# Optimization experiments

Measured on AMD Instinct MI355X. Metric: run time of the kernel, lower is better.

Reference implementation:

```python
import jax, jax.numpy as jnp
import numpy as np


def setup_inputs() -> dict:
    key = jax.random.key(0)
    k1, k2 = jax.random.split(key)
    N, D, C = 65536, 512, 64
    embeddings = jax.random.normal(k1, (N, D), dtype=jnp.float32)
    labels = jax.random.randint(k2, (N,), 0, C, dtype=jnp.int64)
    return {"embeddings": embeddings, "labels": labels, "num_classes": C}


def reference(embeddings, labels, num_classes):
    # Per-class mean (prototypes) via segment reductions. Labels are assumed
    # to be 0..C-1 with all classes present, so unique(labels) == arange(C)
    # and local_labels == labels (faithful to the torch loop in that regime).
    ones = jnp.ones(labels.shape, dtype=embeddings.dtype)
    counts = jax.ops.segment_sum(ones, labels, num_segments=num_classes)  # [C]
    sums = jax.ops.segment_sum(embeddings, labels, num_segments=num_classes)  # [C, D]
    prototypes = sums / counts[:, None]

    # Euclidean cdist: ||e||^2 + ||p||^2 - 2 e.p^T, clamped for numerical safety
    e2 = jnp.sum(embeddings * embeddings, axis=1, keepdims=True)  # [N, 1]
    p2 = jnp.sum(prototypes * prototypes, axis=1)  # [C]
    cross = embeddings @ prototypes.T  # [N, C]
    d2 = jnp.maximum(e2 + p2[None, :] - 2.0 * cross, 1e-12)
    logits = -jnp.sqrt(d2)  # [N, C], negative distances

    log_probs = jax.nn.log_softmax(logits, axis=1)
    n = labels.shape[0]
    nll = -log_probs[jnp.arange(n), labels]
    loss = jnp.mean(nll)
    accuracy = jnp.mean((jnp.argmax(logits, axis=1) == labels).astype(jnp.float32))
    return (loss, accuracy)
```

## Files before the change

kernel.cpp:

```cpp
#include <hip/hip_runtime.h>
#include <math.h>

#define NROWS 65536
#define DIM   512
#define NCLS  64
#define CCAP  1280

typedef __attribute__((ext_vector_type(4))) float f32x4;
typedef __attribute__((ext_vector_type(8))) short s16x8;

#define WS_PROTOSUM 0
#define WS_CURSORS  32768
#define WS_LOSS     32832
#define WS_ACC      32833
#define WS_DONE     32834
#define WS_P2       32836
#define WS_PERM     32912
#define WS_PBF      114944
#define MEMSET_WORDS 32835

static __device__ __forceinline__ unsigned short f2bf(float f) {
    unsigned int u = __float_as_uint(f);
    u += 0x7FFF + ((u >> 16) & 1);
    return (unsigned short)(u >> 16);
}
static __device__ __forceinline__ float bf2f(unsigned short h) {
    return __uint_as_float(((unsigned int)h) << 16);
}

__global__ __launch_bounds__(256) void k_scatter(const int* __restrict__ labels,
                                                 int* __restrict__ cursors,
                                                 int* __restrict__ perm) {
    __shared__ int lh[NCLS], lb[NCLS];
    int t = threadIdx.x;
    if (t < NCLS) lh[t] = 0;
    __syncthreads();
    int i = blockIdx.x * 256 + t;
    int lab = labels[i];
    int rank = atomicAdd(&lh[lab], 1);
    __syncthreads();
    if (t < NCLS) lb[t] = atomicAdd(&cursors[t], lh[t]);
    __syncthreads();
    int pos = lb[lab] + rank;
    if (pos < CCAP) perm[lab * CCAP + pos] = i;
}

__global__ __launch_bounds__(256) void k_psum(const float* __restrict__ emb,
                                              const int* __restrict__ cursors,
                                              const int* __restrict__ perm,
                                              float* __restrict__ protoSum) {
    __shared__ int permS[CCAP];
    __shared__ float4 red[256];
    int t   = threadIdx.x;
    int c   = blockIdx.x >> 5;
    int sub = blockIdx.x & 31;
    int dc  = sub & 3;
    int rs  = sub >> 2;
    int tl  = t & 31;
    int g   = t >> 5;

    int cnt = cursors[c];
    int n = (cnt < CCAP) ? cnt : CCAP;
    for (int i = t; i < n; i += 256) permS[i] = perm[c * CCAP + i];
    __syncthreads();

    const float4* eb = (const float4*)emb + dc * 32 + tl;
    float4 acc = make_float4(0.f, 0.f, 0.f, 0.f);
#pragma unroll 4
    for (int i = rs * 8 + g; i < n; i += 64) {
        int r = permS[i];
        float4 v = eb[(size_t)r * 128];
        acc.x += v.x; acc.y += v.y; acc.z += v.z; acc.w += v.w;
    }
    red[t] = acc;
    __syncthreads();
    if (t < 32) {
        float4 s = red[t];
#pragma unroll
        for (int gg = 1; gg < 8; ++gg) {
            float4 v = red[gg * 32 + t];
            s.x += v.x; s.y += v.y; s.z += v.z; s.w += v.w;
        }
        float* dst = &protoSum[(size_t)c * DIM + dc * 128 + t * 4];
        atomicAdd(dst + 0, s.x);
        atomicAdd(dst + 1, s.y);
        atomicAdd(dst + 2, s.z);
        atomicAdd(dst + 3, s.w);
    }
}

__global__ __launch_bounds__(512) void k_protofin(const float* __restrict__ protoSum,
                                                  const int* __restrict__ cursors,
                                                  unsigned short* __restrict__ pBf,
                                                  float* __restrict__ p2) {
    int c = blockIdx.x, d = threadIdx.x;
    float mean = protoSum[(size_t)c * DIM + d] / (float)cursors[c];
    unsigned short mb = f2bf(mean);
    int kc = d >> 5, quad = (d >> 3) & 3, j = d & 7;
    int nt = c >> 4, l15 = c & 15;
    pBf[(size_t)(((kc * 4 + quad) * 4 + nt) * 16 + l15) * 8 + j] = mb;
    float mf = bf2f(mb);
    float sq = mf * mf;
#pragma unroll
    for (int o = 32; o > 0; o >>= 1) sq += __shfl_down(sq, o, 64);
    __shared__ float red[8];
    if ((d & 63) == 0) red[d >> 6] = sq;
    __syncthreads();
    if (d == 0) {
        float ss = 0.f;
#pragma unroll
        for (int w = 0; w < 8; ++w) ss += red[w];
        p2[c] = ss;
    }
}

#define LROWS 64
#define LGRID (NROWS / LROWS)
__global__ __launch_bounds__(256) void k_logits(const float* __restrict__ emb,
                                                const int* __restrict__ labels,
                                                const unsigned short* __restrict__ pBf,
                                                const float* __restrict__ p2,
                                                float* __restrict__ lossAcc,
                                                float* __restrict__ accAcc,
                                                unsigned int* __restrict__ doneCnt,
                                                float* __restrict__ out) {
    __shared__ float e2s[LROWS];
    __shared__ float rb[8];

    int t    = threadIdx.x;
    int lane = t & 63;
    int wv   = t >> 6;
    int quad = lane >> 4;
    int l15  = lane & 15;
    int rbase = blockIdx.x * LROWS;
    int row   = wv * 16 + l15;

    f32x4 acc[4];
#pragma unroll
    for (int nt = 0; nt < 4; ++nt) acc[nt] = (f32x4){0.f, 0.f, 0.f, 0.f};
    float e2a = 0.f;

    const float4* rp = (const float4*)(emb + (size_t)(rbase + row) * DIM) + quad * 2;
    const s16x8*  bp = (const s16x8*)pBf + quad * 64 + l15;

#pragma unroll 4
    for (int kc = 0; kc < 16; ++kc) {
        float4 g0 = rp[kc * 8];
        float4 g1 = rp[kc * 8 + 1];
        e2a += g0.x * g0.x + g0.y * g0.y + g0.z * g0.z + g0.w * g0.w
             + g1.x * g1.x + g1.y * g1.y + g1.z * g1.z + g1.w * g1.w;
        s16x8 a;
        a[0] = f2bf(g0.x); a[1] = f2bf(g0.y); a[2] = f2bf(g0.z); a[3] = f2bf(g0.w);
        a[4] = f2bf(g1.x); a[5] = f2bf(g1.y); a[6] = f2bf(g1.z); a[7] = f2bf(g1.w);
#pragma unroll
        for (int nt = 0; nt < 4; ++nt) {
            s16x8 b = bp[kc * 256 + nt * 16];
            acc[nt] = __builtin_amdgcn_mfma_f32_16x16x32_bf16(a, b, acc[nt], 0, 0, 0);
        }
    }

    e2a += __shfl_xor(e2a, 16, 64);
    e2a += __shfl_xor(e2a, 32, 64);
    if (quad == 0) e2s[row] = e2a;
    __syncthreads();

    float nlls = 0.f, corr = 0.f;
#pragma unroll
    for (int reg = 0; reg < 4; ++reg) {
        int rloc = wv * 16 + quad * 4 + reg;
        float e2v = e2s[rloc];
        float lg[4];
#pragma unroll
        for (int nt = 0; nt < 4; ++nt) {
            float d2 = e2v + p2[nt * 16 + l15] - 2.f * acc[nt][reg];
            d2 = fmaxf(d2, 1e-12f);
            lg[nt] = -sqrtf(d2);
        }
        float mv = lg[0]; int mc = l15;
#pragma unroll
        for (int nt = 1; nt < 4; ++nt) {
            int cix = nt * 16 + l15;
            if (lg[nt] > mv) { mv = lg[nt]; mc = cix; }
        }
#pragma unroll
        for (int o = 1; o < 16; o <<= 1) {
            float mo = __shfl_xor(mv, o, 64);
            int   co = __shfl_xor(mc, o, 64);
            if (mo > mv || (mo == mv && co < mc)) { mv = mo; mc = co; }
        }
        int lab = labels[rbase + rloc];
        float se = 0.f, ll = 0.f;
#pragma unroll
        for (int nt = 0; nt < 4; ++nt) se += __expf(lg[nt] - mv);
        if ((lab & 15) == l15) ll = lg[lab >> 4];
#pragma unroll
        for (int o = 1; o < 16; o <<= 1) {
            se += __shfl_xor(se, o, 64);
            ll += __shfl_xor(ll, o, 64);
        }
        if (l15 == 0) {
            nlls += __logf(se) + mv - ll;
            corr += (mc == lab) ? 1.f : 0.f;
        }
    }
#pragma unroll
    for (int o = 1; o < 64; o <<= 1) {
        nlls += __shfl_xor(nlls, o, 64);
        corr += __shfl_xor(corr, o, 64);
    }
    if (lane == 0) { rb[wv] = nlls; rb[4 + wv] = corr; }
    __syncthreads();
    if (t == 0) {
        atomicAdd(lossAcc, rb[0] + rb[1] + rb[2] + rb[3]);
        atomicAdd(accAcc, rb[4] + rb[5] + rb[6] + rb[7]);
        __threadfence();
        unsigned int tk = atomicAdd(doneCnt, 1u);
        if (tk == LGRID - 1) {
            float ls  = atomicAdd(lossAcc, 0.f);
            float as_ = atomicAdd(accAcc, 0.f);
            out[0] = ls * (1.f / NROWS);
            out[1] = as_ * (1.f / NROWS);
        }
    }
}

extern "C" void kernel_launch(void* const* d_in, const int* in_sizes, int n_in,
                              void* d_out, int out_size, void* d_ws, size_t ws_size,
                              hipStream_t stream) {
    const float* emb    = (const float*)d_in[0];
    const int*   labels = (const int*)d_in[1];
    float* out = (float*)d_out;

    float* wsf = (float*)d_ws;
    int*   wsi = (int*)d_ws;
    float*          protoSum = wsf + WS_PROTOSUM;
    int*            cursors  = wsi + WS_CURSORS;
    float*          lossAcc  = wsf + WS_LOSS;
    float*          accAcc   = wsf + WS_ACC;
    unsigned int*   doneCnt  = (unsigned int*)(wsi + WS_DONE);
    float*          p2       = wsf + WS_P2;
    int*            perm     = wsi + WS_PERM;
    unsigned short* pBf      = (unsigned short*)(wsf + WS_PBF);

    hipMemsetAsync(d_ws, 0, MEMSET_WORDS * sizeof(int), stream);

    k_scatter<<<NROWS / 256, 256, 0, stream>>>(labels, cursors, perm);
    k_psum<<<NCLS * 32, 256, 0, stream>>>(emb, cursors, perm, protoSum);
    k_protofin<<<NCLS, 512, 0, stream>>>(protoSum, cursors, pBf, p2);
    k_logits<<<LGRID, 256, 0, stream>>>(emb, labels, pBf, p2,
                                        lossAcc, accAcc, doneCnt, out);
}
```

Before: 279.8 us.

## Stream embedding tiles via global_load_lds ring buffer with prefetched prototype fragments

```diff
diff --git a/kernel.cpp b/kernel.cpp
--- a/kernel.cpp
+++ b/kernel.cpp
@@ -26,6 +26,13 @@
 }
 static __device__ __forceinline__ float bf2f(unsigned short h) {
     return __uint_as_float(((unsigned int)h) << 16);
+}
+
+static __device__ __forceinline__ void gll16(const float* g, float* l) {
+    __builtin_amdgcn_global_load_lds(
+        (const __attribute__((address_space(1))) void*)g,
+        (__attribute__((address_space(3))) void*)l,
+        16, 0, 0);
 }
 
 __global__ __launch_bounds__(256) void k_scatter(const int* __restrict__ labels,
@@ -116,7 +123,7 @@
 
 #define LROWS 64
 #define LGRID (NROWS / LROWS)
-__global__ __launch_bounds__(256) void k_logits(const float* __restrict__ emb,
+__global__ __launch_bounds__(256, 4) void k_logits(const float* __restrict__ emb,
                                                 const int* __restrict__ labels,
                                                 const unsigned short* __restrict__ pBf,
                                                 const float* __restrict__ p2,
@@ -124,6 +131,7 @@
                                                 float* __restrict__ accAcc,
                                                 unsigned int* __restrict__ doneCnt,
                                                 float* __restrict__ out) {
+    __shared__ __align__(16) float Ach[4][4][16][32];
     __shared__ float e2s[LROWS];
     __shared__ float rb[8];
 
@@ -133,35 +141,73 @@
     int quad = lane >> 4;
     int l15  = lane & 15;
     int rbase = blockIdx.x * LROWS;
-    int row   = wv * 16 + l15;
 
     f32x4 acc[4];
 #pragma unroll
     for (int nt = 0; nt < 4; ++nt) acc[nt] = (f32x4){0.f, 0.f, 0.f, 0.f};
     float e2a = 0.f;
 
-    const float4* rp = (const float4*)(emb + (size_t)(rbase + row) * DIM) + quad * 2;
-    const s16x8*  bp = (const s16x8*)pBf + quad * 64 + l15;
-
-#pragma unroll 4
+    int drow = lane >> 3;
+    int dcol = 4 * ((lane & 7) ^ drow);
+    const float* gDMA = emb + (size_t)(rbase + wv * 16 + drow) * DIM + dcol;
+    float* ldsW = &Ach[wv][0][0][0];
+
+    int rofs0 = l15 * 32 + (((quad * 2)     ^ (l15 & 7)) << 2);
+    int rofs1 = l15 * 32 + (((quad * 2 + 1) ^ (l15 & 7)) << 2);
+
+    const s16x8* bp = (const s16x8*)pBf + quad * 64 + l15;
+
+    gll16(gDMA,        ldsW);
+    gll16(gDMA + 4096, ldsW + 256);
+    asm volatile("" ::: "memory");
+    s16x8 bcur[4];
+#pragma unroll
+    for (int nt = 0; nt < 4; ++nt) bcur[nt] = bp[nt * 16];
+    asm volatile("" ::: "memory");
+    gll16(gDMA + 32,        ldsW + 512);
+    gll16(gDMA + 32 + 4096, ldsW + 512 + 256);
+    gll16(gDMA + 64,        ldsW + 1024);
+    gll16(gDMA + 64 + 4096, ldsW + 1024 + 256);
+
+#pragma unroll
     for (int kc = 0; kc < 16; ++kc) {
-        float4 g0 = rp[kc * 8];
-        float4 g1 = rp[kc * 8 + 1];
-        e2a += g0.x * g0.x + g0.y * g0.y + g0.z * g0.z + g0.w * g0.w
-             + g1.x * g1.x + g1.y * g1.y + g1.z * g1.z + g1.w * g1.w;
+        s16x8 bnxt[4];
+        if (kc + 1 < 16) {
+#pragma unroll
+            for (int nt = 0; nt < 4; ++nt) bnxt[nt] = bp[(kc + 1) * 256 + nt * 16];
+        }
+        asm volatile("" ::: "memory");
+        if (kc + 3 < 16) {
+            int s = (kc + 3) & 3;
+            gll16(gDMA + (kc + 3) * 32,        ldsW + s * 512);
+            gll16(gDMA + (kc + 3) * 32 + 4096, ldsW + s * 512 + 256);
+        }
+        if      (kc == 0)  asm volatile("s_waitcnt vmcnt(10)" ::: "memory");
+        else if (kc <= 12) asm volatile("s_waitcnt vmcnt(8)"  ::: "memory");
+        else if (kc == 13) asm volatile("s_waitcnt vmcnt(6)"  ::: "memory");
+        else if (kc == 14) asm volatile("s_waitcnt vmcnt(4)"  ::: "memory");
+        else               asm volatile("s_waitcnt vmcnt(0)"  ::: "memory");
+
+        const float* slot = ldsW + (kc & 3) * 512;
+        float4 a0 = *(const float4*)(slot + rofs0);
+        float4 a1 = *(const float4*)(slot + rofs1);
+        e2a += a0.x * a0.x + a0.y * a0.y + a0.z * a0.z + a0.w * a0.w
+             + a1.x * a1.x + a1.y * a1.y + a1.z * a1.z + a1.w * a1.w;
         s16x8 a;
-        a[0] = f2bf(g0.x); a[1] = f2bf(g0.y); a[2] = f2bf(g0.z); a[3] = f2bf(g0.w);
-        a[4] = f2bf(g1.x); a[5] = f2bf(g1.y); a[6] = f2bf(g1.z); a[7] = f2bf(g1.w);
-#pragma unroll
-        for (int nt = 0; nt < 4; ++nt) {
-            s16x8 b = bp[kc * 256 + nt * 16];
-            acc[nt] = __builtin_amdgcn_mfma_f32_16x16x32_bf16(a, b, acc[nt], 0, 0, 0);
+        a[0] = f2bf(a0.x); a[1] = f2bf(a0.y); a[2] = f2bf(a0.z); a[3] = f2bf(a0.w);
+        a[4] = f2bf(a1.x); a[5] = f2bf(a1.y); a[6] = f2bf(a1.z); a[7] = f2bf(a1.w);
+#pragma unroll
+        for (int nt = 0; nt < 4; ++nt)
+            acc[nt] = __builtin_amdgcn_mfma_f32_16x16x32_bf16(a, bcur[nt], acc[nt], 0, 0, 0);
+        if (kc + 1 < 16) {
+#pragma unroll
+            for (int nt = 0; nt < 4; ++nt) bcur[nt] = bnxt[nt];
         }
     }
 
     e2a += __shfl_xor(e2a, 16, 64);
     e2a += __shfl_xor(e2a, 32, 64);
-    if (quad == 0) e2s[row] = e2a;
+    if (quad == 0) e2s[wv * 16 + l15] = e2a;
     __syncthreads();
 
     float nlls = 0.f, corr = 0.f;
```

Measured after the change: 332.3 us. +18.8%, slower.

## Split K across wave pairs with upfront loads and double-buffered B fragments

Applied to the files above, without the earlier changes.

```diff
diff --git a/kernel.cpp b/kernel.cpp
--- a/kernel.cpp
+++ b/kernel.cpp
@@ -114,7 +114,7 @@
     }
 }
 
-#define LROWS 64
+#define LROWS 32
 #define LGRID (NROWS / LROWS)
 __global__ __launch_bounds__(256) void k_logits(const float* __restrict__ emb,
                                                 const int* __restrict__ labels,
@@ -124,83 +124,123 @@
                                                 float* __restrict__ accAcc,
                                                 unsigned int* __restrict__ doneCnt,
                                                 float* __restrict__ out) {
-    __shared__ float e2s[LROWS];
+    __shared__ float accS[2][64][17];
+    __shared__ float e2sA[32], e2sB[32];
     __shared__ float rb[8];
 
     int t    = threadIdx.x;
     int lane = t & 63;
     int wv   = t >> 6;
+    int rwv  = wv & 1;
+    int kh   = wv >> 1;
     int quad = lane >> 4;
     int l15  = lane & 15;
-    int rbase = blockIdx.x * LROWS;
-    int row   = wv * 16 + l15;
+    int rbase = blockIdx.x * LROWS + rwv * 16;
 
     f32x4 acc[4];
 #pragma unroll
     for (int nt = 0; nt < 4; ++nt) acc[nt] = (f32x4){0.f, 0.f, 0.f, 0.f};
     float e2a = 0.f;
 
-    const float4* rp = (const float4*)(emb + (size_t)(rbase + row) * DIM) + quad * 2;
+    const float4* rp = (const float4*)(emb + (size_t)(rbase + l15) * DIM) + quad * 2;
     const s16x8*  bp = (const s16x8*)pBf + quad * 64 + l15;
-
-#pragma unroll 4
-    for (int kc = 0; kc < 16; ++kc) {
-        float4 g0 = rp[kc * 8];
-        float4 g1 = rp[kc * 8 + 1];
+    int kb = kh * 8;
+
+    s16x8 bcur[4];
+#pragma unroll
+    for (int nt = 0; nt < 4; ++nt) bcur[nt] = bp[(size_t)kb * 256 + nt * 16];
+
+    float4 ga[16];
+#pragma unroll
+    for (int i = 0; i < 8; ++i) {
+        ga[2 * i]     = rp[(kb + i) * 8];
+        ga[2 * i + 1] = rp[(kb + i) * 8 + 1];
+    }
+
+#pragma unroll
+    for (int i = 0; i < 8; ++i) {
+        int kc = kb + i;
+        s16x8 bnxt[4];
+        if (i < 7) {
+#pragma unroll
+            for (int nt = 0; nt < 4; ++nt) bnxt[nt] = bp[(size_t)(kc + 1) * 256 + nt * 16];
+        }
+        float4 g0 = ga[2 * i];
+        float4 g1 = ga[2 * i + 1];
         e2a += g0.x * g0.x + g0.y * g0.y + g0.z * g0.z + g0.w * g0.w
              + g1.x * g1.x + g1.y * g1.y + g1.z * g1.z + g1.w * g1.w;
         s16x8 a;
         a[0] = f2bf(g0.x); a[1] = f2bf(g0.y); a[2] = f2bf(g0.z); a[3] = f2bf(g0.w);
         a[4] = f2bf(g1.x); a[5] = f2bf(g1.y); a[6] = f2bf(g1.z); a[7] = f2bf(g1.w);
 #pragma unroll
-        for (int nt = 0; nt < 4; ++nt) {
-            s16x8 b = bp[kc * 256 + nt * 16];
-            acc[nt] = __builtin_amdgcn_mfma_f32_16x16x32_bf16(a, b, acc[nt], 0, 0, 0);
+        for (int nt = 0; nt < 4; ++nt)
+            acc[nt] = __builtin_amdgcn_mfma_f32_16x16x32_bf16(a, bcur[nt], acc[nt], 0, 0, 0);
+        if (i < 7) {
+#pragma unroll
+            for (int nt = 0; nt < 4; ++nt) bcur[nt] = bnxt[nt];
         }
     }
 
     e2a += __shfl_xor(e2a, 16, 64);
     e2a += __shfl_xor(e2a, 32, 64);
-    if (quad == 0) e2s[row] = e2a;
+    if (quad == 0) {
+        if (kh == 0) e2sA[rwv * 16 + l15] = e2a;
+        else         e2sB[rwv * 16 + l15] = e2a;
+    }
+    if (kh == 1) {
+#pragma unroll
+        for (int nt = 0; nt < 4; ++nt)
+#pragma unroll
+            for (int r = 0; r < 4; ++r)
+                accS[rwv][lane][nt * 4 + r] = acc[nt][r];
+    }
     __syncthreads();
 
     float nlls = 0.f, corr = 0.f;
-#pragma unroll
-    for (int reg = 0; reg < 4; ++reg) {
-        int rloc = wv * 16 + quad * 4 + reg;
-        float e2v = e2s[rloc];
-        float lg[4];
-#pragma unroll
-        for (int nt = 0; nt < 4; ++nt) {
-            float d2 = e2v + p2[nt * 16 + l15] - 2.f * acc[nt][reg];
-            d2 = fmaxf(d2, 1e-12f);
-            lg[nt] = -sqrtf(d2);
-        }
-        float mv = lg[0]; int mc = l15;
-#pragma unroll
-        for (int nt = 1; nt < 4; ++nt) {
-            int cix = nt * 16 + l15;
-            if (lg[nt] > mv) { mv = lg[nt]; mc = cix; }
-        }
-#pragma unroll
-        for (int o = 1; o < 16; o <<= 1) {
-            float mo = __shfl_xor(mv, o, 64);
-            int   co = __shfl_xor(mc, o, 64);
-            if (mo > mv || (mo == mv && co < mc)) { mv = mo; mc = co; }
-        }
-        int lab = labels[rbase + rloc];
-        float se = 0.f, ll = 0.f;
-#pragma unroll
-        for (int nt = 0; nt < 4; ++nt) se += __expf(lg[nt] - mv);
-        if ((lab & 15) == l15) ll = lg[lab >> 4];
-#pragma unroll
-        for (int o = 1; o < 16; o <<= 1) {
-            se += __shfl_xor(se, o, 64);
-            ll += __shfl_xor(ll, o, 64);
-        }
-        if (l15 == 0) {
-            nlls += __logf(se) + mv - ll;
-            corr += (mc == lab) ? 1.f : 0.f;
+    if (kh == 0) {
+#pragma unroll
+        for (int nt = 0; nt < 4; ++nt)
+#pragma unroll
+            for (int r = 0; r < 4; ++r)
+                acc[nt][r] += accS[rwv][lane][nt * 4 + r];
+
+#pragma unroll
+        for (int reg = 0; reg < 4; ++reg) {
+            int rowblk = rwv * 16 + quad * 4 + reg;
+            float e2v = e2sA[rowblk] + e2sB[rowblk];
+            float lg[4];
+#pragma unroll
+            for (int nt = 0; nt < 4; ++nt) {
+                float d2 = e2v + p2[nt * 16 + l15] - 2.f * acc[nt][reg];
+                d2 = fmaxf(d2, 1e-12f);
+                lg[nt] = -sqrtf(d2);
+            }
+            float mv = lg[0]; int mc = l15;
+#pragma unroll
+            for (int nt = 1; nt < 4; ++nt) {
+                int cix = nt * 16 + l15;
+                if (lg[nt] > mv) { mv = lg[nt]; mc = cix; }
+            }
+#pragma unroll
+            for (int o = 1; o < 16; o <<= 1) {
+                float mo = __shfl_xor(mv, o, 64);
+                int   co = __shfl_xor(mc, o, 64);
+                if (mo > mv || (mo == mv && co < mc)) { mv = mo; mc = co; }
+            }
+            int lab = labels[blockIdx.x * LROWS + rowblk];
+            float se = 0.f, ll = 0.f;
+#pragma unroll
+            for (int nt = 0; nt < 4; ++nt) se += __expf(lg[nt] - mv);
+            if ((lab & 15) == l15) ll = lg[lab >> 4];
+#pragma unroll
+            for (int o = 1; o < 16; o <<= 1) {
+                se += __shfl_xor(se, o, 64);
+                ll += __shfl_xor(ll, o, 64);
+            }
+            if (l15 == 0) {
+                nlls += __logf(se) + mv - ll;
+                corr += (mc == lab) ? 1.f : 0.f;
+            }
         }
     }
 #pragma unroll
```

After: 323.0 us. +15.4%, slower.

## Precompute bf16 embeddings and row norms in a prep kernel before logits

Applied to the files above, without the earlier changes.

```diff
diff --git a/kernel.cpp b/kernel.cpp
--- a/kernel.cpp
+++ b/kernel.cpp
@@ -17,6 +17,9 @@
 #define WS_P2       32836
 #define WS_PERM     32912
 #define WS_PBF      114944
+#define WS_E2G      131328
+#define WS_EBF      196864
+#define WS_EXT_BYTES 67896320ULL
 #define MEMSET_WORDS 32835
 
 static __device__ __forceinline__ unsigned short f2bf(float f) {
@@ -114,8 +117,125 @@
     }
 }
 
+__global__ __launch_bounds__(256) void k_prep(const float* __restrict__ emb,
+                                              unsigned short* __restrict__ ebf,
+                                              float* __restrict__ e2g) {
+    int t = threadIdx.x, lane = t & 63, wv = t >> 6;
+    int wid = blockIdx.x * 4 + wv;
+    for (int row = wid; row < NROWS; row += 8192) {
+        const float4* rp = (const float4*)(emb + (size_t)row * DIM) + lane * 2;
+        float4 v0 = rp[0];
+        float4 v1 = rp[1];
+        s16x8 h;
+        h[0] = f2bf(v0.x); h[1] = f2bf(v0.y); h[2] = f2bf(v0.z); h[3] = f2bf(v0.w);
+        h[4] = f2bf(v1.x); h[5] = f2bf(v1.y); h[6] = f2bf(v1.z); h[7] = f2bf(v1.w);
+        *(s16x8*)(ebf + (size_t)row * DIM + lane * 8) = h;
+        float sq = v0.x * v0.x + v0.y * v0.y + v0.z * v0.z + v0.w * v0.w
+                 + v1.x * v1.x + v1.y * v1.y + v1.z * v1.z + v1.w * v1.w;
+#pragma unroll
+        for (int o = 1; o < 64; o <<= 1) sq += __shfl_xor(sq, o, 64);
+        if (lane == 0) e2g[row] = sq;
+    }
+}
+
 #define LROWS 64
 #define LGRID (NROWS / LROWS)
+
+__global__ __launch_bounds__(256, 4) void k_logits2(const unsigned short* __restrict__ ebf,
+                                                 const float* __restrict__ e2g,
+                                                 const int* __restrict__ labels,
+                                                 const unsigned short* __restrict__ pBf,
+                                                 const float* __restrict__ p2,
+                                                 float* __restrict__ lossAcc,
+                                                 float* __restrict__ accAcc,
+                                                 unsigned int* __restrict__ doneCnt,
+                                                 float* __restrict__ out) {
+    __shared__ float rb[8];
+    int t    = threadIdx.x;
+    int lane = t & 63;
+    int wv   = t >> 6;
+    int quad = lane >> 4;
+    int l15  = lane & 15;
+    int rbase = blockIdx.x * LROWS;
+    int row   = wv * 16 + l15;
+
+    f32x4 acc[4];
+#pragma unroll
+    for (int nt = 0; nt < 4; ++nt) acc[nt] = (f32x4){0.f, 0.f, 0.f, 0.f};
+
+    const s16x8* ap = (const s16x8*)(ebf + (size_t)(rbase + row) * DIM) + quad;
+    const s16x8* bp = (const s16x8*)pBf + quad * 64 + l15;
+
+#pragma unroll 4
+    for (int kc = 0; kc < 16; ++kc) {
+        s16x8 a = ap[kc * 4];
+#pragma unroll
+        for (int nt = 0; nt < 4; ++nt) {
+            s16x8 b = bp[(size_t)kc * 256 + nt * 16];
+            acc[nt] = __builtin_amdgcn_mfma_f32_16x16x32_bf16(a, b, acc[nt], 0, 0, 0);
+        }
+    }
+
+    float nlls = 0.f, corr = 0.f;
+#pragma unroll
+    for (int reg = 0; reg < 4; ++reg) {
+        int rloc = wv * 16 + quad * 4 + reg;
+        float e2v = e2g[rbase + rloc];
+        float lg[4];
+#pragma unroll
+        for (int nt = 0; nt < 4; ++nt) {
+            float d2 = e2v + p2[nt * 16 + l15] - 2.f * acc[nt][reg];
+            d2 = fmaxf(d2, 1e-12f);
+            lg[nt] = -sqrtf(d2);
+        }
+        float mv = lg[0]; int mc = l15;
+#pragma unroll
+        for (int nt = 1; nt < 4; ++nt) {
+            int cix = nt * 16 + l15;
+            if (lg[nt] > mv) { mv = lg[nt]; mc = cix; }
+        }
+#pragma unroll
+        for (int o = 1; o < 16; o <<= 1) {
+            float mo = __shfl_xor(mv, o, 64);
+            int   co = __shfl_xor(mc, o, 64);
+            if (mo > mv || (mo == mv && co < mc)) { mv = mo; mc = co; }
+        }
+        int lab = labels[rbase + rloc];
+        float se = 0.f, ll = 0.f;
+#pragma unroll
+        for (int nt = 0; nt < 4; ++nt) se += __expf(lg[nt] - mv);
+        if ((lab & 15) == l15) ll = lg[lab >> 4];
+#pragma unroll
+        for (int o = 1; o < 16; o <<= 1) {
+            se += __shfl_xor(se, o, 64);
+            ll += __shfl_xor(ll, o, 64);
+        }
+        if (l15 == 0) {
+            nlls += __logf(se) + mv - ll;
+            corr += (mc == lab) ? 1.f : 0.f;
+        }
+    }
+#pragma unroll
+    for (int o = 1; o < 64; o <<= 1) {
+        nlls += __shfl_xor(nlls, o, 64);
+        corr += __shfl_xor(corr, o, 64);
+    }
+    if (lane == 0) { rb[wv] = nlls; rb[4 + wv] = corr; }
+    __syncthreads();
+    if (t == 0) {
+        atomicAdd(lossAcc, rb[0] + rb[1] + rb[2] + rb[3]);
+        atomicAdd(accAcc, rb[4] + rb[5] + rb[6] + rb[7]);
+        __threadfence();
+        unsigned int tk = atomicAdd(doneCnt, 1u);
+        if (tk == LGRID - 1) {
+            float ls  = atomicAdd(lossAcc, 0.f);
+            float as_ = atomicAdd(accAcc, 0.f);
+            out[0] = ls * (1.f / NROWS);
+            out[1] = as_ * (1.f / NROWS);
+        }
+    }
+}
+
 __global__ __launch_bounds__(256) void k_logits(const float* __restrict__ emb,
                                                 const int* __restrict__ labels,
                                                 const unsigned short* __restrict__ pBf,
@@ -154,7 +274,7 @@
         a[4] = f2bf(g1.x); a[5] = f2bf(g1.y); a[6] = f2bf(g1.z); a[7] = f2bf(g1.w);
 #pragma unroll
         for (int nt = 0; nt < 4; ++nt) {
-            s16x8 b = bp[kc * 256 + nt * 16];
+            s16x8 b = bp[(size_t)kc * 256 + nt * 16];
             acc[nt] = __builtin_amdgcn_mfma_f32_16x16x32_bf16(a, b, acc[nt], 0, 0, 0);
         }
     }
@@ -241,12 +361,22 @@
     float*          p2       = wsf + WS_P2;
     int*            perm     = wsi + WS_PERM;
     unsigned short* pBf      = (unsigned short*)(wsf + WS_PBF);
+    float*          e2g      = wsf + WS_E2G;
+    unsigned short* ebf      = (unsigned short*)(wsf + WS_EBF);
 
     hipMemsetAsync(d_ws, 0, MEMSET_WORDS * sizeof(int), stream);
 
     k_scatter<<<NROWS / 256, 256, 0, stream>>>(labels, cursors, perm);
-    k_psum<<<NCLS * 32, 256, 0, stream>>>(emb, cursors, perm, protoSum);
-    k_protofin<<<NCLS, 512, 0, stream>>>(protoSum, cursors, pBf, p2);
-    k_logits<<<LGRID, 256, 0, stream>>>(emb, labels, pBf, p2,
-                                        lossAcc, accAcc, doneCnt, out);
-}
+    if (ws_size >= WS_EXT_BYTES) {
+        k_prep<<<2048, 256, 0, stream>>>(emb, ebf, e2g);
+        k_psum<<<NCLS * 32, 256, 0, stream>>>(emb, cursors, perm, protoSum);
+        k_protofin<<<NCLS, 512, 0, stream>>>(protoSum, cursors, pBf, p2);
+        k_logits2<<<LGRID, 256, 0, stream>>>(ebf, e2g, labels, pBf, p2,
+                                             lossAcc, accAcc, doneCnt, out);
+    } else {
+        k_psum<<<NCLS * 32, 256, 0, stream>>>(emb, cursors, perm, protoSum);
+        k_protofin<<<NCLS, 512, 0, stream>>>(protoSum, cursors, pBf, p2);
+        k_logits<<<LGRID, 256, 0, stream>>>(emb, labels, pBf, p2,
+                                            lossAcc, accAcc, doneCnt, out);
+    }
+}
```

New measurement: 293.2 us. +4.8%, slower.
